# Optimization experiments

Measured on AMD Instinct MI355X. Metric: run time of the kernel, lower is better.

## Reference

```python
import jax, jax.numpy as jnp
import numpy as np

APPERTURE = 256
Q_SCALE = 0.06


def setup_inputs() -> dict:
    key = jax.random.key(0)
    ks = jax.random.split(key, 5)
    B, N, D_IN, D_OUT = 4, 4096, 1024, 1024
    std = 1.0 / np.sqrt(D_IN)
    x = jax.random.normal(ks[0], (B, N, D_IN), dtype=jnp.float32)
    Wk = jax.random.normal(ks[1], (D_OUT, D_IN), dtype=jnp.float32) * std
    Wq = jax.random.normal(ks[2], (D_OUT, D_IN), dtype=jnp.float32) * std
    Wv = jax.random.normal(ks[3], (D_OUT, D_IN), dtype=jnp.float32) * std
    Wo = jax.random.normal(ks[4], (D_IN, D_OUT), dtype=jnp.float32) * std
    return {"x": x, "Wk": Wk, "Wq": Wq, "Wv": Wv, "Wo": Wo}


def reference(x, Wk, Wq, Wv, Wo):
    # x: [B, N, D_in]; torch Linear(W) computes x @ W.T
    K = jnp.einsum('bnd,od->bno', x, Wk)          # [B, N, D_out]
    Q = jnp.einsum('bnd,od->bno', x, Wq) * Q_SCALE
    V = jnp.einsum('bnd,od->bno', x, Wv)
    logits = jnp.einsum('bno,bmo->bnm', Q, K)      # [B, N, N]
    N = x.shape[1]
    idx = jnp.arange(N)
    # tril(-a) + triu(a) masks |i-j| >= apperture (keep strict band)
    band_mask = jnp.abs(idx[:, None] - idx[None, :]) >= APPERTURE  # [N, N]
    logits = jnp.where(band_mask[None, :, :], -jnp.inf, logits)
    att_weights = jax.nn.softmax(logits, axis=-1)  # [B, N, N]
    # dropout is identity in eval mode
    # y = (V^T @ weights)^T  ->  y[b,n,:] = sum_m att[b,m,n] * V[b,m,:]
    y = jnp.einsum('bmn,bmo->bno', att_weights, V)
    y = jnp.einsum('bno,io->bni', y, Wo)           # [B, N, D_in]
    return (y, att_weights)
```

## Files before the change

kernel.cpp:

```cpp
#include <hip/hip_runtime.h>
#include <stdint.h>

#define SEQ 4096
#define DM  1024
#define NB  4
#define QSCALE 0.06f

typedef __attribute__((ext_vector_type(8))) short short8;
typedef __attribute__((ext_vector_type(4))) float floatx4;

__device__ __forceinline__ unsigned short f2bf(float f) {
  union { float f; unsigned int u; } v; v.f = f;
  unsigned int u = v.u;
  u += 0x7FFFu + ((u >> 16) & 1u);
  return (unsigned short)(u >> 16);
}

__device__ __forceinline__ void async16(const void* g, void* l) {
  __builtin_amdgcn_global_load_lds(
      (const __attribute__((address_space(1))) void*)g,
      (__attribute__((address_space(3))) void*)l, 16, 0, 0);
}

__global__ void cvt_bf16(const float* __restrict__ in,
                         unsigned short* __restrict__ out, int n) {
  int i = (blockIdx.x * 256 + threadIdx.x) * 8;
  if (i >= n) return;
  const float4* p = (const float4*)(in + i);
  float4 a = p[0], b = p[1];
  short8 o;
  o[0] = (short)f2bf(a.x); o[1] = (short)f2bf(a.y);
  o[2] = (short)f2bf(a.z); o[3] = (short)f2bf(a.w);
  o[4] = (short)f2bf(b.x); o[5] = (short)f2bf(b.y);
  o[6] = (short)f2bf(b.z); o[7] = (short)f2bf(b.w);
  *(short8*)(out + i) = o;
}

__global__ void cvt_w4(const float* __restrict__ wk, const float* __restrict__ wq,
                       const float* __restrict__ wv, const float* __restrict__ wo,
                       unsigned short* __restrict__ out) {
  int blk = blockIdx.x;
  int sel = blk >> 9;
  const float* src = sel == 0 ? wk : sel == 1 ? wq : sel == 2 ? wv : wo;
  int i = ((blk & 511) * 256 + threadIdx.x) * 8;
  const float4* p = (const float4*)(src + i);
  float4 a = p[0], b = p[1];
  short8 o;
  o[0] = (short)f2bf(a.x); o[1] = (short)f2bf(a.y);
  o[2] = (short)f2bf(a.z); o[3] = (short)f2bf(a.w);
  o[4] = (short)f2bf(b.x); o[5] = (short)f2bf(b.y);
  o[6] = (short)f2bf(b.z); o[7] = (short)f2bf(b.w);
  *(short8*)(out + sel * 1048576 + i) = o;
}

template <bool OUT_BF16, int MT, int NT, bool DUAL>
__global__ __launch_bounds__(512, 2) void gemm256(
    const unsigned short* __restrict__ A, const unsigned short* __restrict__ W,
    void* __restrict__ C0, void* __restrict__ C1, float a0, float a1, long ldc) {
  __shared__ __align__(16) unsigned short lds[4 * 16384];
  const int K = 1024;
  const int NKT = 32;
  int tid = threadIdx.x;
  int lane = tid & 63;
  int wid = tid >> 6;
  int wr = wid >> 2, wc = wid & 3;

  const int CPX = (MT * NT) >> 3;
  int bid = blockIdx.x;
  int raw = (bid & 7) * CPX + (bid >> 3);
  int bx = raw % MT;
  int by = raw / MT;
  long brow = (long)bx * 256;
  long bcol = (long)by * 256;

  floatx4 acc[8][4];
#pragma unroll
  for (int i = 0; i < 8; i++)
#pragma unroll
    for (int j = 0; j < 4; j++) acc[i][j] = (floatx4){0.f, 0.f, 0.f, 0.f};

  const unsigned short* Ag = A + (brow + (tid >> 2)) * K + (tid & 3) * 8;
  const unsigned short* Wg = W + (bcol + (tid >> 2)) * K + (tid & 3) * 8;
  unsigned short* ldsW = lds + wid * 512;

  int aRd = (wr * 128 + (lane & 15)) * 32 + (lane >> 4) * 8;
  int bRd = (wc * 64 + (lane & 15)) * 32 + (lane >> 4) * 8;

#pragma unroll
  for (int tt = 0; tt < 3; tt++) {
    unsigned short* d = ldsW + tt * 16384;
    const unsigned short* a = Ag + tt * 32;
    const unsigned short* w = Wg + tt * 32;
    async16(a, d);
    async16(a + 128 * K, d + 4096);
    async16(w, d + 8192);
    async16(w + 128 * K, d + 12288);
  }
  asm volatile("s_waitcnt vmcnt(8)" ::: "memory");
  __builtin_amdgcn_s_barrier();

  for (int t = 0; t < NKT; ++t) {
    const unsigned short* bufA = lds + (t & 3) * 16384;
    const unsigned short* bufB = bufA + 8192;
    short8 a0f[4], b0f[4], a1f[4];
#pragma unroll
    for (int mt = 0; mt < 4; mt++)
      a0f[mt] = *(const short8*)(bufA + aRd + mt * 512);
#pragma unroll
    for (int nt = 0; nt < 4; nt++)
      b0f[nt] = *(const short8*)(bufB + bRd + nt * 512);
    if (t + 3 < NKT) {
      unsigned short* d = ldsW + ((t + 3) & 3) * 16384;
      const unsigned short* a = Ag + (t + 3) * 32;
      async16(a, d);
      async16(a + 128 * K, d + 4096);
    }
    __builtin_amdgcn_s_barrier();
    __builtin_amdgcn_s_setprio(1);
#pragma unroll
    for (int mt = 0; mt < 4; mt++)
#pragma unroll
      for (int nt = 0; nt < 4; nt++)
        acc[mt][nt] = __builtin_amdgcn_mfma_f32_16x16x32_bf16(
            a0f[mt], b0f[nt], acc[mt][nt], 0, 0, 0);
    __builtin_amdgcn_s_setprio(0);
    __builtin_amdgcn_s_barrier();
#pragma unroll
    for (int mt = 0; mt < 4; mt++)
      a1f[mt] = *(const short8*)(bufA + aRd + 2048 + mt * 512);
    if (t + 3 < NKT) {
      unsigned short* d = ldsW + ((t + 3) & 3) * 16384;
      const unsigned short* w = Wg + (t + 3) * 32;
      async16(w, d + 8192);
      async16(w + 128 * K, d + 12288);
    }
    __builtin_amdgcn_s_barrier();
    __builtin_amdgcn_s_setprio(1);
#pragma unroll
    for (int mt = 0; mt < 4; mt++)
#pragma unroll
      for (int nt = 0; nt < 4; nt++)
        acc[4 + mt][nt] = __builtin_amdgcn_mfma_f32_16x16x32_bf16(
            a1f[mt], b0f[nt], acc[4 + mt][nt], 0, 0, 0);
    __builtin_amdgcn_s_setprio(0);
    if (t < NKT - 3)
      asm volatile("s_waitcnt vmcnt(8)" ::: "memory");
    else if (t == NKT - 3)
      asm volatile("s_waitcnt vmcnt(4)" ::: "memory");
    else
      asm volatile("s_waitcnt vmcnt(0)" ::: "memory");
    __builtin_amdgcn_s_barrier();
  }

  void* Cp;
  float alpha;
  long cc;
  if (DUAL && by >= NT / 2) {
    Cp = C1; alpha = a1; cc = bcol - (long)(NT / 2) * 256;
  } else {
    Cp = C0; alpha = a0; cc = bcol;
  }
  long crow = brow + wr * 128 + (lane >> 4) * 4;
  long ccol = cc + wc * 64 + (lane & 15);
#pragma unroll
  for (int mt = 0; mt < 8; mt++)
#pragma unroll
    for (int nt = 0; nt < 4; nt++)
#pragma unroll
      for (int r = 0; r < 4; r++) {
        float v = acc[mt][nt][r] * alpha;
        long idx = (crow + mt * 16 + r) * ldc + ccol + nt * 16;
        if (OUT_BF16)
          ((unsigned short*)Cp)[idx] = f2bf(v);
        else
          ((float*)Cp)[idx] = v;
      }
}

__global__ __launch_bounds__(256) void attn_logits(
    const unsigned short* __restrict__ Qb, const unsigned short* __restrict__ Kb,
    float* __restrict__ att) {
  int b = blockIdx.z;
  int n0 = blockIdx.y * 128;
  int m0 = n0 - 256 + blockIdx.x * 128;
  if (m0 + 128 <= 0 || m0 >= SEQ) return;
  __shared__ unsigned short sA[128 * 32];
  __shared__ unsigned short sB[128 * 32];
  const int K = 1024;
  int tid = threadIdx.x;
  int wid = tid >> 6, lane = tid & 63;
  int wr = wid >> 1, wc = wid & 1;

  floatx4 acc[4][4];
#pragma unroll
  for (int i = 0; i < 4; i++)
#pragma unroll
    for (int j = 0; j < 4; j++) acc[i][j] = (floatx4){0.f, 0.f, 0.f, 0.f};

  int c0 = wid * 64 + lane;
  int c1 = c0 + 256;
  const unsigned short* Qbase = Qb + (long)b * SEQ * K;
  const unsigned short* Kbase = Kb + (long)b * SEQ * K;
  int br0 = m0 + (c0 >> 2); br0 = br0 < 0 ? 0 : (br0 > SEQ - 1 ? SEQ - 1 : br0);
  int br1 = m0 + (c1 >> 2); br1 = br1 < 0 ? 0 : (br1 > SEQ - 1 ? SEQ - 1 : br1);
  const unsigned short* Ag0 = Qbase + (long)(n0 + (c0 >> 2)) * K + (c0 & 3) * 8;
  const unsigned short* Ag1 = Qbase + (long)(n0 + (c1 >> 2)) * K + (c1 & 3) * 8;
  const unsigned short* Bg0 = Kbase + (long)br0 * K + (c0 & 3) * 8;
  const unsigned short* Bg1 = Kbase + (long)br1 * K + (c1 & 3) * 8;
  unsigned short* sA0 = sA + (wid * 64) * 8;
  unsigned short* sA1 = sA + (256 + wid * 64) * 8;
  unsigned short* sB0 = sB + (wid * 64) * 8;
  unsigned short* sB1 = sB + (256 + wid * 64) * 8;

  int aRd = (wr * 64 + (lane & 15)) * 32 + (lane >> 4) * 8;
  int bRd = (wc * 64 + (lane & 15)) * 32 + (lane >> 4) * 8;

  for (int ks = 0; ks < K; ks += 32) {
    async16(Ag0 + ks, sA0);
    async16(Ag1 + ks, sA1);
    async16(Bg0 + ks, sB0);
    async16(Bg1 + ks, sB1);
    __syncthreads();
    short8 af[4], bf[4];
#pragma unroll
    for (int mt = 0; mt < 4; mt++) af[mt] = *(const short8*)(sA + aRd + mt * 512);
#pragma unroll
    for (int nt = 0; nt < 4; nt++) bf[nt] = *(const short8*)(sB + bRd + nt * 512);
#pragma unroll
    for (int mt = 0; mt < 4; mt++)
#pragma unroll
      for (int nt = 0; nt < 4; nt++)
        acc[mt][nt] = __builtin_amdgcn_mfma_f32_16x16x32_bf16(
            af[mt], bf[nt], acc[mt][nt], 0, 0, 0);
    __syncthreads();
  }

  float* attB = att + (long)b * SEQ * SEQ;
  int crow = n0 + wr * 64 + (lane >> 4) * 4;
  int ccol = m0 + wc * 64 + (lane & 15);
#pragma unroll
  for (int mt = 0; mt < 4; mt++)
#pragma unroll
    for (int nt = 0; nt < 4; nt++)
#pragma unroll
      for (int r = 0; r < 4; r++) {
        int row = crow + mt * 16 + r;
        int col = ccol + nt * 16;
        int d = row - col;
        if (col >= 0 && col < SEQ && d < 256 && d > -256)
          attB[(long)row * SEQ + col] = acc[mt][nt][r];
      }
}

__global__ __launch_bounds__(256) void softmax_band(
    float* __restrict__ att, unsigned short* __restrict__ attT2) {
  __shared__ float e_lds[16 * 545];
  __shared__ float inv_s[16];
  int blk = blockIdx.x;
  int b = blk >> 8;
  int r0 = (blk & 255) * 16;
  int tid = threadIdx.x;
  int row = tid >> 4;
  int t16 = tid & 15;
  int i = r0 + row;
  int jbase = r0 - 272;
  float* arow = att + ((long)b * SEQ + i) * (long)SEQ;

  float raw[34];
  float m = -1e30f;
#pragma unroll
  for (int s = 0; s < 34; s++) {
    int jj = s * 16 + t16;
    int j = jbase + jj;
    bool ok = (j >= 0) && (j < SEQ) && (j >= i - 255) && (j <= i + 255);
    float v = ok ? arow[j] : -1e30f;
    raw[s] = v;
    m = fmaxf(m, v);
  }
#pragma unroll
  for (int off = 8; off; off >>= 1) m = fmaxf(m, __shfl_xor(m, off, 16));

  float sum = 0.f;
#pragma unroll
  for (int s = 0; s < 34; s++) {
    int jj = s * 16 + t16;
    float e = (raw[s] > -1e29f) ? __expf(raw[s] - m) : 0.f;
    e_lds[row * 545 + jj] = e;
    sum += e;
  }
#pragma unroll
  for (int off = 8; off; off >>= 1) sum += __shfl_xor(sum, off, 16);
  float invr = 1.0f / sum;
  if (t16 == 0) inv_s[row] = invr;
  __syncthreads();

  for (int s = 0; s < 64; s++) {
    int j0 = (s * 16 + t16) * 4;
    float4 w;
    float* wp = (float*)&w;
#pragma unroll
    for (int k = 0; k < 4; k++) {
      int j = j0 + k;
      bool ok = (j >= i - 255) && (j <= i + 255);
      int jj = j - jbase;
      jj = jj < 0 ? 0 : (jj > 543 ? 543 : jj);
      wp[k] = ok ? e_lds[row * 545 + jj] * invr : 0.f;
    }
    *(float4*)(arow + j0) = w;
  }

  int nn = tid >> 4;
  int mi16 = tid & 15;
  int i2 = r0 + mi16;
  float inv2 = inv_s[mi16];
  int Bc = r0 & ~255;
  for (int s = 0; s < 48; s++) {
    int n = Bc - 256 + s * 16 + nn;
    if (n < 0 || n >= SEQ) continue;
    int mi = i2 - (n & ~255) + 256;
    bool ok = (n >= i2 - 255) && (n <= i2 + 255);
    int jj = n - jbase;
    jj = jj < 0 ? 0 : (jj > 544 ? 544 : jj);
    float val = ok ? e_lds[mi16 * 545 + jj] * inv2 : 0.f;
    attT2[(((long)b * 16 + (n >> 8)) * 256 + (n & 255)) * 768 + mi] = f2bf(val);
  }
}

__global__ __launch_bounds__(512, 2) void attv256(
    const unsigned short* __restrict__ attT2, const unsigned short* __restrict__ Vt,
    unsigned short* __restrict__ yb) {
  __shared__ __align__(16) unsigned short lds[4 * 16384];
  const int KA = 768;
  const int NKT = 24;
  int b = blockIdx.z;
  int nb2 = blockIdx.x;
  int o0 = blockIdx.y * 256;
  int N0 = nb2 * 256;
  int tid = threadIdx.x;
  int lane = tid & 63;
  int wid = tid >> 6;
  int wr = wid >> 2, wc = wid & 3;

  floatx4 acc[8][4];
#pragma unroll
  for (int i = 0; i < 8; i++)
#pragma unroll
    for (int j = 0; j < 4; j++) acc[i][j] = (floatx4){0.f, 0.f, 0.f, 0.f};

  const unsigned short* Abase = attT2 + ((long)(b * 16 + nb2) * 256) * KA;
  const unsigned short* Ag = Abase + (long)(tid >> 2) * KA + (tid & 3) * 8;
  const unsigned short* Vg =
      Vt + (long)(o0 + (tid >> 2)) * (NB * SEQ) + (tid & 3) * 8;
  unsigned short* ldsW = lds + wid * 512;

  int aRd = (wr * 128 + (lane & 15)) * 32 + (lane >> 4) * 8;
  int bRd = (wc * 64 + (lane & 15)) * 32 + (lane >> 4) * 8;

  auto boff = [&](int t) {
    int mg = N0 - 256 + t * 32;
    int mc = mg < 0 ? 0 : (mg > SEQ - 32 ? SEQ - 32 : mg);
    return (long)b * SEQ + mc;
  };

#pragma unroll
  for (int tt = 0; tt < 3; tt++) {
    unsigned short* d = ldsW + tt * 16384;
    async16(Ag + tt * 32, d);
    async16(Ag + 128 * KA + tt * 32, d + 4096);
    long bo = boff(tt);
    async16(Vg + bo, d + 8192);
    async16(Vg + 128L * (NB * SEQ) + bo, d + 12288);
  }
  asm volatile("s_waitcnt vmcnt(8)" ::: "memory");
  __builtin_amdgcn_s_barrier();

  for (int t = 0; t < NKT; ++t) {
    const unsigned short* bufA = lds + (t & 3) * 16384;
    const unsigned short* bufB = bufA + 8192;
    short8 a0f[4], b0f[4], a1f[4];
#pragma unroll
    for (int mt = 0; mt < 4; mt++)
      a0f[mt] = *(const short8*)(bufA + aRd + mt * 512);
#pragma unroll
    for (int nt = 0; nt < 4; nt++)
      b0f[nt] = *(const short8*)(bufB + bRd + nt * 512);
    if (t + 3 < NKT) {
      unsigned short* d = ldsW + ((t + 3) & 3) * 16384;
      async16(Ag + (t + 3) * 32, d);
      async16(Ag + 128 * KA + (t + 3) * 32, d + 4096);
    }
    __builtin_amdgcn_s_barrier();
    __builtin_amdgcn_s_setprio(1);
#pragma unroll
    for (int mt = 0; mt < 4; mt++)
#pragma unroll
      for (int nt = 0; nt < 4; nt++)
        acc[mt][nt] = __builtin_amdgcn_mfma_f32_16x16x32_bf16(
            a0f[mt], b0f[nt], acc[mt][nt], 0, 0, 0);
    __builtin_amdgcn_s_setprio(0);
    __builtin_amdgcn_s_barrier();
#pragma unroll
    for (int mt = 0; mt < 4; mt++)
      a1f[mt] = *(const short8*)(bufA + aRd + 2048 + mt * 512);
    if (t + 3 < NKT) {
      unsigned short* d = ldsW + ((t + 3) & 3) * 16384;
      long bo = boff(t + 3);
      async16(Vg + bo, d + 8192);
      async16(Vg + 128L * (NB * SEQ) + bo, d + 12288);
    }
    __builtin_amdgcn_s_barrier();
    __builtin_amdgcn_s_setprio(1);
#pragma unroll
    for (int mt = 0; mt < 4; mt++)
#pragma unroll
      for (int nt = 0; nt < 4; nt++)
        acc[4 + mt][nt] = __builtin_amdgcn_mfma_f32_16x16x32_bf16(
            a1f[mt], b0f[nt], acc[4 + mt][nt], 0, 0, 0);
    __builtin_amdgcn_s_setprio(0);
    if (t < NKT - 3)
      asm volatile("s_waitcnt vmcnt(8)" ::: "memory");
    else if (t == NKT - 3)
      asm volatile("s_waitcnt vmcnt(4)" ::: "memory");
    else
      asm volatile("s_waitcnt vmcnt(0)" ::: "memory");
    __builtin_amdgcn_s_barrier();
  }

  long crow = (long)b * SEQ + N0 + wr * 128 + (lane >> 4) * 4;
  int ccol = o0 + wc * 64 + (lane & 15);
#pragma unroll
  for (int mt = 0; mt < 8; mt++)
#pragma unroll
    for (int nt = 0; nt < 4; nt++)
#pragma unroll
      for (int r = 0; r < 4; r++)
        yb[(crow + mt * 16 + r) * DM + ccol + nt * 16] = f2bf(acc[mt][nt][r]);
}

extern "C" void kernel_launch(void* const* d_in, const int* in_sizes, int n_in,
                              void* d_out, int out_size, void* d_ws, size_t ws_size,
                              hipStream_t stream) {
  const float* x  = (const float*)d_in[0];
  const float* Wk = (const float*)d_in[1];
  const float* Wq = (const float*)d_in[2];
  const float* Wv = (const float*)d_in[3];
  const float* Wo = (const float*)d_in[4];
  float* outY = (float*)d_out;
  float* outAtt = outY + (long)NB * SEQ * DM;

  char* ws = (char*)d_ws;
  unsigned short* xb  = (unsigned short*)(ws + 0);
  unsigned short* Kb  = (unsigned short*)(ws + 33554432);
  unsigned short* Qb  = (unsigned short*)(ws + 67108864);
  unsigned short* Vt  = (unsigned short*)(ws + 100663296);
  unsigned short* Wkb = (unsigned short*)(ws + 134217728);
  unsigned short* Wvb = Wkb + 2097152;
  unsigned short* Wob = Wvb + 1048576;
  unsigned short* attT2 = Kb;
  unsigned short* yb = xb;

  cvt_bf16<<<8192, 256, 0, stream>>>(x, xb, NB * SEQ * DM);
  cvt_w4<<<2048, 256, 0, stream>>>(Wk, Wq, Wv, Wo, Wkb);

  gemm256<true, 64, 8, true><<<512, 512, 0, stream>>>(
      xb, Wkb, Kb, Qb, 1.0f, QSCALE, 1024);
  gemm256<true, 4, 64, false><<<256, 512, 0, stream>>>(
      Wvb, xb, Vt, nullptr, 1.0f, 1.0f, NB * SEQ);

  attn_logits<<<dim3(5, 32, NB), 256, 0, stream>>>(Qb, Kb, outAtt);
  hipMemsetAsync(attT2, 0, (size_t)NB * 16 * 256 * 768 * 2, stream);
  softmax_band<<<1024, 256, 0, stream>>>(outAtt, attT2);
  attv256<<<dim3(16, 4, NB), 512, 0, stream>>>(attT2, Vt, yb);
  gemm256<false, 64, 4, false><<<256, 512, 0, stream>>>(
      yb, Wob, outY, nullptr, 1.0f, 1.0f, 1024);
}
```

Baseline: 666.4 us.

## Merge conversion kernels, retile banded logits to 256, skip dead attv tiles, drop memset

Merges the activation and weight bf16 conversion kernels into one launch. Rewrites the banded QK^T logits kernel to use 256x256 tiles with the same 4-stage async-LDS pipelined MFMA schedule as the projection GEMMs, replacing the 128x128 single-buffered version. The attention-times-V kernel now skips MFMA work on K-slices outside the sequence, and the memset that zeroed the transposed attention buffer is removed. The risk is correctness if softmax_band does not write every entry that attv reads, and the larger tiles compute more out-of-band products.

```diff
diff --git a/kernel.cpp b/kernel.cpp
--- a/kernel.cpp
+++ b/kernel.cpp
@@ -22,27 +22,23 @@
       (__attribute__((address_space(3))) void*)l, 16, 0, 0);
 }
 
-__global__ void cvt_bf16(const float* __restrict__ in,
-                         unsigned short* __restrict__ out, int n) {
-  int i = (blockIdx.x * 256 + threadIdx.x) * 8;
-  if (i >= n) return;
-  const float4* p = (const float4*)(in + i);
-  float4 a = p[0], b = p[1];
-  short8 o;
-  o[0] = (short)f2bf(a.x); o[1] = (short)f2bf(a.y);
-  o[2] = (short)f2bf(a.z); o[3] = (short)f2bf(a.w);
-  o[4] = (short)f2bf(b.x); o[5] = (short)f2bf(b.y);
-  o[6] = (short)f2bf(b.z); o[7] = (short)f2bf(b.w);
-  *(short8*)(out + i) = o;
-}
-
-__global__ void cvt_w4(const float* __restrict__ wk, const float* __restrict__ wq,
-                       const float* __restrict__ wv, const float* __restrict__ wo,
-                       unsigned short* __restrict__ out) {
+__global__ void cvt_all(const float* __restrict__ x, const float* __restrict__ wk,
+                        const float* __restrict__ wq, const float* __restrict__ wv,
+                        const float* __restrict__ wo, unsigned short* __restrict__ xb,
+                        unsigned short* __restrict__ wb) {
   int blk = blockIdx.x;
-  int sel = blk >> 9;
-  const float* src = sel == 0 ? wk : sel == 1 ? wq : sel == 2 ? wv : wo;
-  int i = ((blk & 511) * 256 + threadIdx.x) * 8;
+  const float* src;
+  unsigned short* dst;
+  int i;
+  if (blk < 8192) {
+    src = x; dst = xb; i = (blk * 256 + threadIdx.x) * 8;
+  } else {
+    int w = blk - 8192;
+    int sel = w >> 9;
+    src = sel == 0 ? wk : sel == 1 ? wq : sel == 2 ? wv : wo;
+    dst = wb + sel * 1048576;
+    i = ((w & 511) * 256 + threadIdx.x) * 8;
+  }
   const float4* p = (const float4*)(src + i);
   float4 a = p[0], b = p[1];
   short8 o;
@@ -50,7 +46,7 @@
   o[2] = (short)f2bf(a.z); o[3] = (short)f2bf(a.w);
   o[4] = (short)f2bf(b.x); o[5] = (short)f2bf(b.y);
   o[6] = (short)f2bf(b.z); o[7] = (short)f2bf(b.w);
-  *(short8*)(out + sel * 1048576 + i) = o;
+  *(short8*)(dst + i) = o;
 }
 
 template <bool OUT_BF16, int MT, int NT, bool DUAL>
@@ -177,69 +173,107 @@
       }
 }
 
-__global__ __launch_bounds__(256) void attn_logits(
+__global__ __launch_bounds__(512, 2) void logits256(
     const unsigned short* __restrict__ Qb, const unsigned short* __restrict__ Kb,
     float* __restrict__ att) {
   int b = blockIdx.z;
-  int n0 = blockIdx.y * 128;
-  int m0 = n0 - 256 + blockIdx.x * 128;
-  if (m0 + 128 <= 0 || m0 >= SEQ) return;
-  __shared__ unsigned short sA[128 * 32];
-  __shared__ unsigned short sB[128 * 32];
+  int n0 = blockIdx.x * 256;
+  int m0 = n0 + ((int)blockIdx.y - 1) * 256;
+  if (m0 < 0 || m0 >= SEQ) return;
+  __shared__ __align__(16) unsigned short lds[4 * 16384];
   const int K = 1024;
+  const int NKT = 32;
   int tid = threadIdx.x;
-  int wid = tid >> 6, lane = tid & 63;
-  int wr = wid >> 1, wc = wid & 1;
-
-  floatx4 acc[4][4];
-#pragma unroll
-  for (int i = 0; i < 4; i++)
+  int lane = tid & 63;
+  int wid = tid >> 6;
+  int wr = wid >> 2, wc = wid & 3;
+
+  floatx4 acc[8][4];
+#pragma unroll
+  for (int i = 0; i < 8; i++)
 #pragma unroll
     for (int j = 0; j < 4; j++) acc[i][j] = (floatx4){0.f, 0.f, 0.f, 0.f};
 
-  int c0 = wid * 64 + lane;
-  int c1 = c0 + 256;
-  const unsigned short* Qbase = Qb + (long)b * SEQ * K;
-  const unsigned short* Kbase = Kb + (long)b * SEQ * K;
-  int br0 = m0 + (c0 >> 2); br0 = br0 < 0 ? 0 : (br0 > SEQ - 1 ? SEQ - 1 : br0);
-  int br1 = m0 + (c1 >> 2); br1 = br1 < 0 ? 0 : (br1 > SEQ - 1 ? SEQ - 1 : br1);
-  const unsigned short* Ag0 = Qbase + (long)(n0 + (c0 >> 2)) * K + (c0 & 3) * 8;
-  const unsigned short* Ag1 = Qbase + (long)(n0 + (c1 >> 2)) * K + (c1 & 3) * 8;
-  const unsigned short* Bg0 = Kbase + (long)br0 * K + (c0 & 3) * 8;
-  const unsigned short* Bg1 = Kbase + (long)br1 * K + (c1 & 3) * 8;
-  unsigned short* sA0 = sA + (wid * 64) * 8;
-  unsigned short* sA1 = sA + (256 + wid * 64) * 8;
-  unsigned short* sB0 = sB + (wid * 64) * 8;
-  unsigned short* sB1 = sB + (256 + wid * 64) * 8;
-
-  int aRd = (wr * 64 + (lane & 15)) * 32 + (lane >> 4) * 8;
+  const unsigned short* Ag =
+      Qb + ((long)b * SEQ + n0 + (tid >> 2)) * K + (tid & 3) * 8;
+  const unsigned short* Wg =
+      Kb + ((long)b * SEQ + m0 + (tid >> 2)) * K + (tid & 3) * 8;
+  unsigned short* ldsW = lds + wid * 512;
+
+  int aRd = (wr * 128 + (lane & 15)) * 32 + (lane >> 4) * 8;
   int bRd = (wc * 64 + (lane & 15)) * 32 + (lane >> 4) * 8;
 
-  for (int ks = 0; ks < K; ks += 32) {
-    async16(Ag0 + ks, sA0);
-    async16(Ag1 + ks, sA1);
-    async16(Bg0 + ks, sB0);
-    async16(Bg1 + ks, sB1);
-    __syncthreads();
-    short8 af[4], bf[4];
-#pragma unroll
-    for (int mt = 0; mt < 4; mt++) af[mt] = *(const short8*)(sA + aRd + mt * 512);
-#pragma unroll
-    for (int nt = 0; nt < 4; nt++) bf[nt] = *(const short8*)(sB + bRd + nt * 512);
+#pragma unroll
+  for (int tt = 0; tt < 3; tt++) {
+    unsigned short* d = ldsW + tt * 16384;
+    const unsigned short* a = Ag + tt * 32;
+    const unsigned short* w = Wg + tt * 32;
+    async16(a, d);
+    async16(a + 128 * K, d + 4096);
+    async16(w, d + 8192);
+    async16(w + 128 * K, d + 12288);
+  }
+  asm volatile("s_waitcnt vmcnt(8)" ::: "memory");
+  __builtin_amdgcn_s_barrier();
+
+  for (int t = 0; t < NKT; ++t) {
+    const unsigned short* bufA = lds + (t & 3) * 16384;
+    const unsigned short* bufB = bufA + 8192;
+    short8 a0f[4], b0f[4], a1f[4];
+#pragma unroll
+    for (int mt = 0; mt < 4; mt++)
+      a0f[mt] = *(const short8*)(bufA + aRd + mt * 512);
+#pragma unroll
+    for (int nt = 0; nt < 4; nt++)
+      b0f[nt] = *(const short8*)(bufB + bRd + nt * 512);
+    if (t + 3 < NKT) {
+      unsigned short* d = ldsW + ((t + 3) & 3) * 16384;
+      const unsigned short* a = Ag + (t + 3) * 32;
+      async16(a, d);
+      async16(a + 128 * K, d + 4096);
+    }
+    __builtin_amdgcn_s_barrier();
+    __builtin_amdgcn_s_setprio(1);
 #pragma unroll
     for (int mt = 0; mt < 4; mt++)
 #pragma unroll
       for (int nt = 0; nt < 4; nt++)
         acc[mt][nt] = __builtin_amdgcn_mfma_f32_16x16x32_bf16(
-            af[mt], bf[nt], acc[mt][nt], 0, 0, 0);
-    __syncthreads();
+            a0f[mt], b0f[nt], acc[mt][nt], 0, 0, 0);
+    __builtin_amdgcn_s_setprio(0);
+    __builtin_amdgcn_s_barrier();
+#pragma unroll
+    for (int mt = 0; mt < 4; mt++)
+      a1f[mt] = *(const short8*)(bufA + aRd + 2048 + mt * 512);
+    if (t + 3 < NKT) {
+      unsigned short* d = ldsW + ((t + 3) & 3) * 16384;
+      const unsigned short* w = Wg + (t + 3) * 32;
+      async16(w, d + 8192);
+      async16(w + 128 * K, d + 12288);
+    }
+    __builtin_amdgcn_s_barrier();
+    __builtin_amdgcn_s_setprio(1);
+#pragma unroll
+    for (int mt = 0; mt < 4; mt++)
+#pragma unroll
+      for (int nt = 0; nt < 4; nt++)
+        acc[4 + mt][nt] = __builtin_amdgcn_mfma_f32_16x16x32_bf16(
+            a1f[mt], b0f[nt], acc[4 + mt][nt], 0, 0, 0);
+    __builtin_amdgcn_s_setprio(0);
+    if (t < NKT - 3)
+      asm volatile("s_waitcnt vmcnt(8)" ::: "memory");
+    else if (t == NKT - 3)
+      asm volatile("s_waitcnt vmcnt(4)" ::: "memory");
+    else
+      asm volatile("s_waitcnt vmcnt(0)" ::: "memory");
+    __builtin_amdgcn_s_barrier();
   }
 
   float* attB = att + (long)b * SEQ * SEQ;
-  int crow = n0 + wr * 64 + (lane >> 4) * 4;
+  int crow = n0 + wr * 128 + (lane >> 4) * 4;
   int ccol = m0 + wc * 64 + (lane & 15);
 #pragma unroll
-  for (int mt = 0; mt < 4; mt++)
+  for (int mt = 0; mt < 8; mt++)
 #pragma unroll
     for (int nt = 0; nt < 4; nt++)
 #pragma unroll
@@ -247,7 +281,7 @@
         int row = crow + mt * 16 + r;
         int col = ccol + nt * 16;
         int d = row - col;
-        if (col >= 0 && col < SEQ && d < 256 && d > -256)
+        if (d < 256 && d > -256)
           attB[(long)row * SEQ + col] = acc[mt][nt][r];
       }
 }
@@ -375,6 +409,8 @@
   __builtin_amdgcn_s_barrier();
 
   for (int t = 0; t < NKT; ++t) {
+    int mg = N0 - 256 + t * 32;
+    bool live = (mg > -32) && (mg < SEQ);
     const unsigned short* bufA = lds + (t & 3) * 16384;
     const unsigned short* bufB = bufA + 8192;
     short8 a0f[4], b0f[4], a1f[4];
@@ -390,14 +426,16 @@
       async16(Ag + 128 * KA + (t + 3) * 32, d + 4096);
     }
     __builtin_amdgcn_s_barrier();
-    __builtin_amdgcn_s_setprio(1);
-#pragma unroll
-    for (int mt = 0; mt < 4; mt++)
-#pragma unroll
-      for (int nt = 0; nt < 4; nt++)
-        acc[mt][nt] = __builtin_amdgcn_mfma_f32_16x16x32_bf16(
-            a0f[mt], b0f[nt], acc[mt][nt], 0, 0, 0);
-    __builtin_amdgcn_s_setprio(0);
+    if (live) {
+      __builtin_amdgcn_s_setprio(1);
+#pragma unroll
+      for (int mt = 0; mt < 4; mt++)
+#pragma unroll
+        for (int nt = 0; nt < 4; nt++)
+          acc[mt][nt] = __builtin_amdgcn_mfma_f32_16x16x32_bf16(
+              a0f[mt], b0f[nt], acc[mt][nt], 0, 0, 0);
+      __builtin_amdgcn_s_setprio(0);
+    }
     __builtin_amdgcn_s_barrier();
 #pragma unroll
     for (int mt = 0; mt < 4; mt++)
@@ -409,14 +447,16 @@
       async16(Vg + 128L * (NB * SEQ) + bo, d + 12288);
     }
     __builtin_amdgcn_s_barrier();
-    __builtin_amdgcn_s_setprio(1);
-#pragma unroll
-    for (int mt = 0; mt < 4; mt++)
-#pragma unroll
-      for (int nt = 0; nt < 4; nt++)
-        acc[4 + mt][nt] = __builtin_amdgcn_mfma_f32_16x16x32_bf16(
-            a1f[mt], b0f[nt], acc[4 + mt][nt], 0, 0, 0);
-    __builtin_amdgcn_s_setprio(0);
+    if (live) {
+      __builtin_amdgcn_s_setprio(1);
+#pragma unroll
+      for (int mt = 0; mt < 4; mt++)
+#pragma unroll
+        for (int nt = 0; nt < 4; nt++)
+          acc[4 + mt][nt] = __builtin_amdgcn_mfma_f32_16x16x32_bf16(
+              a1f[mt], b0f[nt], acc[4 + mt][nt], 0, 0, 0);
+      __builtin_amdgcn_s_setprio(0);
+    }
     if (t < NKT - 3)
       asm volatile("s_waitcnt vmcnt(8)" ::: "memory");
     else if (t == NKT - 3)
@@ -459,16 +499,14 @@
   unsigned short* attT2 = Kb;
   unsigned short* yb = xb;
 
-  cvt_bf16<<<8192, 256, 0, stream>>>(x, xb, NB * SEQ * DM);
-  cvt_w4<<<2048, 256, 0, stream>>>(Wk, Wq, Wv, Wo, Wkb);
+  cvt_all<<<10240, 256, 0, stream>>>(x, Wk, Wq, Wv, Wo, xb, Wkb);
 
   gemm256<true, 64, 8, true><<<512, 512, 0, stream>>>(
       xb, Wkb, Kb, Qb, 1.0f, QSCALE, 1024);
   gemm256<true, 4, 64, false><<<256, 512, 0, stream>>>(
       Wvb, xb, Vt, nullptr, 1.0f, 1.0f, NB * SEQ);
 
-  attn_logits<<<dim3(5, 32, NB), 256, 0, stream>>>(Qb, Kb, outAtt);
-  hipMemsetAsync(attT2, 0, (size_t)NB * 16 * 256 * 768 * 2, stream);
+  logits256<<<dim3(16, 3, NB), 512, 0, stream>>>(Qb, Kb, outAtt);
   softmax_band<<<1024, 256, 0, stream>>>(outAtt, attT2);
   attv256<<<dim3(16, 4, NB), 512, 0, stream>>>(attT2, Vt, yb);
   gemm256<false, 64, 4, false><<<256, 512, 0, stream>>>(
```

Measured after the change: 640.0 us. -4.0%, faster.
